# Optimization experiments

Hardware: AMD Instinct MI355X
Metric: run time of the kernel (lower is better)

## Reference

```python
import jax, jax.numpy as jnp
import numpy as np

B, S, D, H = 2, 2048, 1024, 16
DK = D // H  # 64


def rotate_half(x):
    d = x.shape[-1]
    x1, x2 = x[..., : d // 2], x[..., d // 2 :]
    return jnp.concatenate([-x2, x1], axis=-1)


def apply_rope(q, k):
    # q, k: [B, H, S, DK]
    d_k = q.shape[-1]
    seq_len = q.shape[-2]
    theta = 10000.0 ** (-2.0 / d_k * jnp.arange(d_k // 2, dtype=q.dtype))
    positions = jnp.arange(seq_len, dtype=q.dtype)
    angles = jnp.outer(positions, theta)                    # [S, DK/2]
    cos = jnp.tile(jnp.cos(angles), (1, 2))                 # [S, DK]
    sin = jnp.tile(jnp.sin(angles), (1, 2))
    q = q * cos + rotate_half(q) * sin
    k = k * cos + rotate_half(k) * sin
    return q, k


def setup_inputs() -> dict:
    key = jax.random.key(0)
    ks = jax.random.split(key, 9)
    std = 1.0 / np.sqrt(D)
    x = jax.random.normal(ks[0], (B, S, D), dtype=jnp.float32)
    # mask True = masked (code uses masked_fill(mask, -inf)); causal mask
    mask = jnp.triu(jnp.ones((S, S), dtype=bool), k=1)[None, None, :, :]
    mask = jnp.broadcast_to(mask, (B, 1, S, S))
    Wq = jax.random.uniform(ks[1], (D, D), jnp.float32, -std, std)
    bq = jax.random.uniform(ks[2], (D,), jnp.float32, -std, std)
    Wk = jax.random.uniform(ks[3], (D, D), jnp.float32, -std, std)
    bk = jax.random.uniform(ks[4], (D,), jnp.float32, -std, std)
    Wv = jax.random.uniform(ks[5], (D, D), jnp.float32, -std, std)
    bv = jax.random.uniform(ks[6], (D,), jnp.float32, -std, std)
    Wo = jax.random.uniform(ks[7], (D, D), jnp.float32, -std, std)
    bo = jax.random.uniform(ks[8], (D,), jnp.float32, -std, std)
    return {"x": x, "mask": mask, "Wq": Wq, "bq": bq, "Wk": Wk, "bk": bk,
            "Wv": Wv, "bv": bv, "Wo": Wo, "bo": bo}


def reference(x, mask, Wq, bq, Wk, bk, Wv, bv, Wo, bo):
    b, s, d = x.shape
    # projections -> [B, H, S, DK]
    q = (x @ Wq + bq).reshape(b, s, H, DK).transpose(0, 2, 1, 3)
    k = (x @ Wk + bk).reshape(b, s, H, DK).transpose(0, 2, 1, 3)
    v = (x @ Wv + bv).reshape(b, s, H, DK).transpose(0, 2, 1, 3)
    q, k = apply_rope(q, k)
    scores = jnp.einsum("bhqd,bhkd->bhqk", q, k) / np.sqrt(DK)
    scores = jnp.where(mask, -jnp.inf, scores)
    probs = jax.nn.softmax(scores, axis=-1)
    attn = jnp.einsum("bhqk,bhkd->bhqd", probs, v)
    o = attn.transpose(0, 2, 1, 3).reshape(b, s, H * DK)
    return o @ Wo + bo
```

## Files before the change

kernel.cpp:

```cpp
#include <hip/hip_runtime.h>
#include <hip/hip_bf16.h>
#include <math.h>

typedef __hip_bfloat16 bf16;
typedef __attribute__((ext_vector_type(8))) short short8;
typedef __attribute__((ext_vector_type(4))) short s16x4;
typedef __attribute__((ext_vector_type(4))) float f32x4;

#define B_  2
#define S_  2048
#define D_  1024
#define H_  16
#define DK_ 64

#define QSCALE 0.18033688011112043f
#define EXPOFF 11.541560327111707f

__device__ inline short bfs(float f) { return __builtin_bit_cast(short, __float2bfloat16(f)); }

#define GLL16(gptr, lptr)                                                        \
    __builtin_amdgcn_global_load_lds(                                            \
        (const __attribute__((address_space(1))) void*)(gptr),                   \
        (__attribute__((address_space(3))) void*)(lptr), 16, 0, 0)

#if __has_builtin(__builtin_amdgcn_mfma_f32_16x16x16bf16_1k)
#define MFMA_16x16x16(A, Bv, C) __builtin_amdgcn_mfma_f32_16x16x16bf16_1k(A, Bv, C, 0, 0, 0)
#elif __has_builtin(__builtin_amdgcn_mfma_f32_16x16x16_bf16)
#define MFMA_16x16x16(A, Bv, C) __builtin_amdgcn_mfma_f32_16x16x16_bf16(A, Bv, C, 0, 0, 0)
#else
static __device__ inline f32x4 mfma16_asm(s16x4 a, s16x4 b, f32x4 c) {
    f32x4 d;
    asm volatile("v_mfma_f32_16x16x16_bf16 %0, %1, %2, %3\n\ts_nop 7\n\ts_nop 7"
                 : "=v"(d) : "v"(a), "v"(b), "v"(c));
    return d;
}
#define MFMA_16x16x16(A, Bv, C) mfma16_asm(A, Bv, C)
#endif

__global__ __launch_bounds__(256)
void prep_k(const float* __restrict__ x,
            const float* __restrict__ W0, const float* __restrict__ W1,
            const float* __restrict__ W2, const float* __restrict__ W3,
            bf16* __restrict__ cx, bf16* __restrict__ Wt)
{
    const int z = blockIdx.z;
    const int t = threadIdx.x;
    if (z == 4) {
        const int bid = blockIdx.y * 16 + blockIdx.x;
        #pragma unroll
        for (int i = 0; i < 16; i++) {
            const size_t g = ((size_t)bid * 256 + t) * 4 + (size_t)i * 262144;
            const float4 v = *(const float4*)(x + g);
            s16x4 o = { bfs(v.x), bfs(v.y), bfs(v.z), bfs(v.w) };
            *(s16x4*)(cx + g) = o;
        }
        return;
    }
    __shared__ float Lt[64][65];
    const float* W = (z == 0) ? W0 : (z == 1) ? W1 : (z == 2) ? W2 : W3;
    bf16* dst = Wt + (size_t)z * D_ * D_;
    const int k0 = blockIdx.y * 64, n0 = blockIdx.x * 64;
    #pragma unroll
    for (int p = 0; p < 4; p++) {
        const int idx = p * 256 + t;
        const int row = idx >> 4, cb = (idx & 15) * 4;
        const float4 v = *(const float4*)(W + (size_t)(k0 + row) * D_ + n0 + cb);
        Lt[cb + 0][row] = v.x; Lt[cb + 1][row] = v.y;
        Lt[cb + 2][row] = v.z; Lt[cb + 3][row] = v.w;
    }
    __syncthreads();
    #pragma unroll
    for (int p = 0; p < 4; p++) {
        const int idx = p * 256 + t;
        const int n = idx >> 4, kb = (idx & 15) * 4;
        s16x4 o = { bfs(Lt[n][kb]), bfs(Lt[n][kb + 1]), bfs(Lt[n][kb + 2]), bfs(Lt[n][kb + 3]) };
        *(s16x4*)(dst + (size_t)(n0 + n) * D_ + k0 + kb) = o;
    }
}

template<int MODE, int TM>
__global__ __launch_bounds__(256)
void gemm_k(const bf16* __restrict__ A, const bf16* __restrict__ WtAll,
            const float* __restrict__ b0, const float* __restrict__ b1,
            const float* __restrict__ b2,
            bf16* __restrict__ d0, bf16* __restrict__ d1, bf16* __restrict__ d2,
            float* __restrict__ fout)
{
    constexpr int K = D_;
    constexpr int MT = (B_ * S_) / TM;
    constexpr int AI = TM / 64;
    const int L = (int)blockIdx.x;
    const int m0 = (L & (MT - 1)) * TM;
    const int rest = L / MT;
    const int z = (MODE == 0) ? (rest >> 4) : 3;
    const int n0 = (MODE == 0) ? (rest & 15) * 64 : rest * 64;
    const bf16* W = WtAll + (size_t)z * D_ * D_;
    const float* bias = (MODE == 1) ? b0 : ((z == 0) ? b0 : (z == 1) ? b1 : b2);

    __shared__ __align__(16) short As[TM * 32];
    __shared__ __align__(16) short Bs[64 * 32];

    const int t = threadIdx.x;
    const int wave = t >> 6, lane = t & 63, quad = lane >> 4, l16 = lane & 15;
    const int wm = wave * (TM / 4);

    const bf16* gA0 = A + (size_t)(m0 + (t >> 2)) * K + (t & 3) * 8;
    const bf16* gA1 = gA0 + (size_t)64 * K;
    const bf16* gW0 = W + (size_t)(n0 + (t >> 2)) * K + (t & 3) * 8;
    const int wb = wave * 512;

    f32x4 acc[AI][4] = {};

    for (int k0 = 0; k0 < K; k0 += 32) {
        __syncthreads();
        GLL16(gA0 + k0, &As[wb]);
        if (TM == 128) GLL16(gA1 + k0, &As[2048 + wb]);
        GLL16(gW0 + k0, &Bs[wb]);
        __syncthreads();
        short8 af[AI], bf[4];
        #pragma unroll
        for (int i = 0; i < AI; i++) af[i] = *(const short8*)&As[(wm + i * 16 + l16) * 32 + quad * 8];
        #pragma unroll
        for (int j = 0; j < 4; j++) bf[j] = *(const short8*)&Bs[(j * 16 + l16) * 32 + quad * 8];
        #pragma unroll
        for (int i = 0; i < AI; i++)
            #pragma unroll
            for (int j = 0; j < 4; j++)
                acc[i][j] = __builtin_amdgcn_mfma_f32_16x16x32_bf16(af[i], bf[j], acc[i][j], 0, 0, 0);
    }

    if (MODE == 1) {
        #pragma unroll
        for (int j = 0; j < 4; j++) {
            const int ncol = n0 + j * 16 + l16;
            const float bb = bias[ncol];
            #pragma unroll
            for (int i = 0; i < AI; i++) {
                const int mbase = m0 + wm + i * 16 + quad * 4;
                #pragma unroll
                for (int r = 0; r < 4; r++)
                    fout[(size_t)(mbase + r) * D_ + ncol] = acc[i][j][r] + bb;
            }
        }
    } else if (z == 2) {
        const int h = n0 >> 6;
        #pragma unroll
        for (int j = 0; j < 4; j++) {
            const int ncol = n0 + j * 16 + l16;
            const float bb = bias[ncol];
            const int dk = ncol & 63;
            #pragma unroll
            for (int i = 0; i < AI; i++) {
                const int mbase = m0 + wm + i * 16 + quad * 4;
                #pragma unroll
                for (int r = 0; r < 4; r++) {
                    const int m = mbase + r;
                    const int b = m >> 11, s = m & (S_ - 1);
                    d2[(((size_t)(b * H_ + h)) * DK_ + dk) * S_ + s] = __float2bfloat16(acc[i][j][r] + bb);
                }
            }
        }
    } else {
        bf16* dst = z ? d1 : d0;
        const float sc = z ? 1.0f : QSCALE;
        const int h = n0 >> 6;
        #pragma unroll
        for (int j = 0; j < 2; j++) {
            const int dk = j * 16 + l16;
            const float th = exp2f((float)dk * -0.41524101186092029f);
            const float blo = bias[(h << 6) + dk];
            const float bhi = bias[(h << 6) + dk + 32];
            #pragma unroll
            for (int i = 0; i < AI; i++) {
                #pragma unroll
                for (int r = 0; r < 4; r++) {
                    const int m = m0 + wm + i * 16 + quad * 4 + r;
                    const int b = m >> 11, s = m & (S_ - 1);
                    float sn, cs;
                    sincosf((float)s * th, &sn, &cs);
                    const float v1 = acc[i][j][r] + blo;
                    const float v2 = acc[i][j + 2][r] + bhi;
                    bf16* p = dst + (((size_t)(b * H_ + h)) * S_ + s) * DK_;
                    p[dk]      = __float2bfloat16((v1 * cs - v2 * sn) * sc);
                    p[dk + 32] = __float2bfloat16((v2 * cs + v1 * sn) * sc);
                }
            }
        }
    }
}

template<bool DIAG>
__device__ __forceinline__
void attn_tile(const short* __restrict__ Ks, const short* __restrict__ Vts,
               const short8 qf0, const short8 qf1,
               f32x4* ot, float& l_acc,
               const int wave, const int quad, const int l16)
{
    const int kkmax = DIAG ? wave : 3;
    #pragma unroll
    for (int kk = 0; kk <= kkmax; kk++) {
        const short8 kf0 = *(const short8*)&Ks[(kk * 16 + l16) * 72 + quad * 8];
        const short8 kf1 = *(const short8*)&Ks[(kk * 16 + l16) * 72 + 32 + quad * 8];
        f32x4 st = {};
        st = __builtin_amdgcn_mfma_f32_16x16x32_bf16(kf0, qf0, st, 0, 0, 0);
        st = __builtin_amdgcn_mfma_f32_16x16x32_bf16(kf1, qf1, st, 0, 0, 0);

        s16x4 pt;
        float psum = 0.0f;
        #pragma unroll
        for (int r = 0; r < 4; r++) {
            float p;
            if (DIAG) {
                const bool masked = (kk == wave) && (quad * 4 + r > l16);
                p = masked ? 0.0f : exp2f(st[r] - EXPOFF);
            } else {
                p = exp2f(st[r] - EXPOFF);
            }
            psum += p;
            pt[r] = bfs(p);
        }
        l_acc += psum;

        #pragma unroll
        for (int dt = 0; dt < 4; dt++) {
            const s16x4 vf = *(const s16x4*)&Vts[(dt * 16 + l16) * 72 + kk * 16 + quad * 4];
            ot[dt] = MFMA_16x16x16(vf, pt, ot[dt]);
        }
    }
}

__global__ __launch_bounds__(256)
void attn_k(const bf16* __restrict__ q_ws, const bf16* __restrict__ k_ws,
            const bf16* __restrict__ vt_ws, bf16* __restrict__ attn_ws)
{
    __shared__ __align__(16) short Ks[2][64 * 72];
    __shared__ __align__(16) short Vts[2][64 * 72];

    const int linear = (int)blockIdx.y * 16 + (int)blockIdx.x;
    const int bh = linear & 31;
    const int pr = linear >> 5;
    const int qtA = pr, qtB = 31 - pr;
    const int t = threadIdx.x;
    const int wave = t >> 6, quad = (t & 63) >> 4, l16 = t & 15;
    const bf16* Kb = k_ws + (size_t)bh * S_ * DK_;
    const bf16* Vb = vt_ws + (size_t)bh * DK_ * S_;
    const int b = bh >> 4, h = bh & 15;

    const bf16* QbA = q_ws + ((size_t)bh * S_ + qtA * 64 + wave * 16) * DK_;
    const bf16* QbB = q_ws + ((size_t)bh * S_ + qtB * 64 + wave * 16) * DK_;
    const short8 qfA0 = *(const short8*)(QbA + (size_t)l16 * DK_ + quad * 8);
    const short8 qfA1 = *(const short8*)(QbA + (size_t)l16 * DK_ + 32 + quad * 8);
    const short8 qfB0 = *(const short8*)(QbB + (size_t)l16 * DK_ + quad * 8);
    const short8 qfB1 = *(const short8*)(QbB + (size_t)l16 * DK_ + 32 + quad * 8);

    float lA = 0.0f, lB = 0.0f;
    f32x4 otA[4] = {}, otB[4] = {};

    for (int kt0 = 0; kt0 <= qtB; kt0 += 2) {
        const int kt1 = kt0 + 1;
        const bool has1 = (kt1 <= qtB);
        __syncthreads();
        #pragma unroll
        for (int p = 0; p < 2; p++) {
            const int idx = p * 256 + t;
            const int row = idx >> 3, cb = (idx & 7) * 8;
            *(float4*)&Ks[0][row * 72 + cb]  = *(const float4*)(Kb + (size_t)(kt0 * 64 + row) * DK_ + cb);
            *(float4*)&Vts[0][row * 72 + cb] = *(const float4*)(Vb + (size_t)row * S_ + kt0 * 64 + cb);
        }
        if (has1) {
            #pragma unroll
            for (int p = 0; p < 2; p++) {
                const int idx = p * 256 + t;
                const int row = idx >> 3, cb = (idx & 7) * 8;
                *(float4*)&Ks[1][row * 72 + cb]  = *(const float4*)(Kb + (size_t)(kt1 * 64 + row) * DK_ + cb);
                *(float4*)&Vts[1][row * 72 + cb] = *(const float4*)(Vb + (size_t)row * S_ + kt1 * 64 + cb);
            }
        }
        __syncthreads();

        if (kt0 == qtB) attn_tile<true >(Ks[0], Vts[0], qfB0, qfB1, otB, lB, wave, quad, l16);
        else            attn_tile<false>(Ks[0], Vts[0], qfB0, qfB1, otB, lB, wave, quad, l16);
        if (has1) {
            if (kt1 == qtB) attn_tile<true >(Ks[1], Vts[1], qfB0, qfB1, otB, lB, wave, quad, l16);
            else            attn_tile<false>(Ks[1], Vts[1], qfB0, qfB1, otB, lB, wave, quad, l16);
        }
        if (kt0 <= qtA) {
            if (kt0 == qtA) attn_tile<true >(Ks[0], Vts[0], qfA0, qfA1, otA, lA, wave, quad, l16);
            else            attn_tile<false>(Ks[0], Vts[0], qfA0, qfA1, otA, lA, wave, quad, l16);
        }
        if (has1 && kt1 <= qtA) {
            if (kt1 == qtA) attn_tile<true >(Ks[1], Vts[1], qfA0, qfA1, otA, lA, wave, quad, l16);
            else            attn_tile<false>(Ks[1], Vts[1], qfA0, qfA1, otA, lA, wave, quad, l16);
        }
    }

    #pragma unroll
    for (int which = 0; which < 2; which++) {
        float l_acc = which ? lB : lA;
        f32x4* ot = which ? otB : otA;
        const int q0 = (which ? qtB : qtA) * 64;
        l_acc += __shfl_xor(l_acc, 16, 64);
        l_acc += __shfl_xor(l_acc, 32, 64);
        const float inv = 1.0f / l_acc;
        const int srow = q0 + wave * 16 + l16;
        bf16* orow = attn_ws + ((size_t)(b * S_ + srow)) * D_ + h * 64;
        #pragma unroll
        for (int dt = 0; dt < 4; dt++) {
            s16x4 o4 = { bfs(ot[dt][0] * inv), bfs(ot[dt][1] * inv),
                         bfs(ot[dt][2] * inv), bfs(ot[dt][3] * inv) };
            *(s16x4*)(orow + dt * 16 + quad * 4) = o4;
        }
    }
}

extern "C" void kernel_launch(void* const* d_in, const int* in_sizes, int n_in,
                              void* d_out, int out_size, void* d_ws, size_t ws_size,
                              hipStream_t stream)
{
    (void)out_size; (void)ws_size;
    const float* x = nullptr;
    const float* W[4] = {nullptr, nullptr, nullptr, nullptr};
    const float* bias[4] = {nullptr, nullptr, nullptr, nullptr};
    int wi = 0, bi = 0;
    for (int i = 0; i < n_in; i++) {
        const int sz = in_sizes[i];
        if (sz == B_ * S_ * D_ && x == nullptr) x = (const float*)d_in[i];
        else if (sz == D_ * D_ && wi < 4) W[wi++] = (const float*)d_in[i];
        else if (sz == D_ && bi < 4) bias[bi++] = (const float*)d_in[i];
    }

    bf16* ws = (bf16*)d_ws;
    const size_t SEG = (size_t)B_ * S_ * D_;
    bf16* canonX  = ws;
    bf16* Wt      = ws + SEG;
    bf16* k_ws    = ws + 2 * SEG;
    bf16* vt_ws   = ws + 3 * SEG;
    bf16* attn_ws = canonX;
    bf16* q_ws    = (bf16*)d_out;

    prep_k<<<dim3(16, 16, 5), 256, 0, stream>>>(x, W[0], W[1], W[2], W[3], canonX, Wt);

    gemm_k<0, 128><<<dim3(1536, 1, 1), 256, 0, stream>>>(
        canonX, Wt, bias[0], bias[1], bias[2], q_ws, k_ws, vt_ws, nullptr);

    attn_k<<<dim3(16, 32), 256, 0, stream>>>(q_ws, k_ws, vt_ws, attn_ws);

    gemm_k<1, 64><<<dim3(1024, 1, 1), 256, 0, stream>>>(
        attn_ws, Wt, bias[3], nullptr, nullptr, nullptr, nullptr, nullptr,
        (float*)d_out);
}
```

Baseline: 218.6 us.

## Retile GEMMs to 128xTN blocks and split attention into one q-tile per block

The projection GEMM now uses 128x128 tiles, with waves arranged 2x2 so each wave covers one head. The output GEMM uses 128x64 tiles, which halves the grid sizes and improves operand reuse per block. The attention kernel drops the paired q-tile scheme and gives each block a single q-tile. It orders tiles longest-first within groups, with bh on blockIdx.x. This doubles the attention grid to raise parallelism, but each block now loads K/V for only one query tile, so K/V reuse drops and the scheduler must balance the causal load.

```diff
diff --git a/kernel.cpp b/kernel.cpp
--- a/kernel.cpp
+++ b/kernel.cpp
@@ -78,7 +78,7 @@
     }
 }
 
-template<int MODE, int TM>
+template<int MODE, int TN>
 __global__ __launch_bounds__(256)
 void gemm_k(const bf16* __restrict__ A, const bf16* __restrict__ WtAll,
             const float* __restrict__ b0, const float* __restrict__ b1,
@@ -87,25 +87,30 @@
             float* __restrict__ fout)
 {
     constexpr int K = D_;
+    constexpr int TM = 128;
     constexpr int MT = (B_ * S_) / TM;
-    constexpr int AI = TM / 64;
+    constexpr int NT = D_ / TN;
+    constexpr int WAVES_N = TN / 64;
+    constexpr int WM = TM / (4 / WAVES_N);
+    constexpr int AI = WM / 16;
+
     const int L = (int)blockIdx.x;
     const int m0 = (L & (MT - 1)) * TM;
-    const int rest = L / MT;
-    const int z = (MODE == 0) ? (rest >> 4) : 3;
-    const int n0 = (MODE == 0) ? (rest & 15) * 64 : rest * 64;
+    const int rest = L >> 5;
+    const int z = (MODE == 0) ? (rest >> 3) : 3;
+    const int n0 = (MODE == 0) ? (rest & (NT - 1)) * TN : rest * TN;
     const bf16* W = WtAll + (size_t)z * D_ * D_;
     const float* bias = (MODE == 1) ? b0 : ((z == 0) ? b0 : (z == 1) ? b1 : b2);
 
     __shared__ __align__(16) short As[TM * 32];
-    __shared__ __align__(16) short Bs[64 * 32];
+    __shared__ __align__(16) short Bs[TN * 32];
 
     const int t = threadIdx.x;
     const int wave = t >> 6, lane = t & 63, quad = lane >> 4, l16 = lane & 15;
-    const int wm = wave * (TM / 4);
+    const int wr = (WAVES_N == 2) ? (wave >> 1) : wave;
+    const int wc = (WAVES_N == 2) ? (wave & 1) : 0;
 
     const bf16* gA0 = A + (size_t)(m0 + (t >> 2)) * K + (t & 3) * 8;
-    const bf16* gA1 = gA0 + (size_t)64 * K;
     const bf16* gW0 = W + (size_t)(n0 + (t >> 2)) * K + (t & 3) * 8;
     const int wb = wave * 512;
 
@@ -114,44 +119,44 @@
     for (int k0 = 0; k0 < K; k0 += 32) {
         __syncthreads();
         GLL16(gA0 + k0, &As[wb]);
-        if (TM == 128) GLL16(gA1 + k0, &As[2048 + wb]);
+        GLL16(gA0 + (size_t)64 * K + k0, &As[2048 + wb]);
         GLL16(gW0 + k0, &Bs[wb]);
+        if (TN == 128) GLL16(gW0 + (size_t)64 * K + k0, &Bs[2048 + wb]);
         __syncthreads();
-        short8 af[AI], bf[4];
-        #pragma unroll
-        for (int i = 0; i < AI; i++) af[i] = *(const short8*)&As[(wm + i * 16 + l16) * 32 + quad * 8];
-        #pragma unroll
-        for (int j = 0; j < 4; j++) bf[j] = *(const short8*)&Bs[(j * 16 + l16) * 32 + quad * 8];
+        short8 af[AI], bfv[4];
+        #pragma unroll
+        for (int i = 0; i < AI; i++) af[i] = *(const short8*)&As[(wr * WM + i * 16 + l16) * 32 + quad * 8];
+        #pragma unroll
+        for (int j = 0; j < 4; j++) bfv[j] = *(const short8*)&Bs[(wc * 64 + j * 16 + l16) * 32 + quad * 8];
         #pragma unroll
         for (int i = 0; i < AI; i++)
             #pragma unroll
             for (int j = 0; j < 4; j++)
-                acc[i][j] = __builtin_amdgcn_mfma_f32_16x16x32_bf16(af[i], bf[j], acc[i][j], 0, 0, 0);
+                acc[i][j] = __builtin_amdgcn_mfma_f32_16x16x32_bf16(af[i], bfv[j], acc[i][j], 0, 0, 0);
     }
 
     if (MODE == 1) {
         #pragma unroll
         for (int j = 0; j < 4; j++) {
-            const int ncol = n0 + j * 16 + l16;
+            const int ncol = n0 + wc * 64 + j * 16 + l16;
             const float bb = bias[ncol];
             #pragma unroll
             for (int i = 0; i < AI; i++) {
-                const int mbase = m0 + wm + i * 16 + quad * 4;
+                const int mbase = m0 + wr * WM + i * 16 + quad * 4;
                 #pragma unroll
                 for (int r = 0; r < 4; r++)
                     fout[(size_t)(mbase + r) * D_ + ncol] = acc[i][j][r] + bb;
             }
         }
     } else if (z == 2) {
-        const int h = n0 >> 6;
+        const int h = (n0 >> 6) + wc;
         #pragma unroll
         for (int j = 0; j < 4; j++) {
-            const int ncol = n0 + j * 16 + l16;
-            const float bb = bias[ncol];
-            const int dk = ncol & 63;
+            const int dk = j * 16 + l16;
+            const float bb = bias[(h << 6) + dk];
             #pragma unroll
             for (int i = 0; i < AI; i++) {
-                const int mbase = m0 + wm + i * 16 + quad * 4;
+                const int mbase = m0 + wr * WM + i * 16 + quad * 4;
                 #pragma unroll
                 for (int r = 0; r < 4; r++) {
                     const int m = mbase + r;
@@ -163,7 +168,7 @@
     } else {
         bf16* dst = z ? d1 : d0;
         const float sc = z ? 1.0f : QSCALE;
-        const int h = n0 >> 6;
+        const int h = (n0 >> 6) + wc;
         #pragma unroll
         for (int j = 0; j < 2; j++) {
             const int dk = j * 16 + l16;
@@ -174,7 +179,7 @@
             for (int i = 0; i < AI; i++) {
                 #pragma unroll
                 for (int r = 0; r < 4; r++) {
-                    const int m = m0 + wm + i * 16 + quad * 4 + r;
+                    const int m = m0 + wr * WM + i * 16 + quad * 4 + r;
                     const int b = m >> 11, s = m & (S_ - 1);
                     float sn, cs;
                     sincosf((float)s * th, &sn, &cs);
@@ -236,29 +241,27 @@
     __shared__ __align__(16) short Ks[2][64 * 72];
     __shared__ __align__(16) short Vts[2][64 * 72];
 
-    const int linear = (int)blockIdx.y * 16 + (int)blockIdx.x;
-    const int bh = linear & 31;
-    const int pr = linear >> 5;
-    const int qtA = pr, qtB = 31 - pr;
+    const int bh = (int)blockIdx.x;
+    const int by = (int)blockIdx.y;
+    const int j8 = by & 7, g = by >> 3;
+    const int qt = (g == 0) ? (31 - j8) : (g == 1) ? j8 : (g == 2) ? (23 - j8) : (8 + j8);
+
     const int t = threadIdx.x;
     const int wave = t >> 6, quad = (t & 63) >> 4, l16 = t & 15;
     const bf16* Kb = k_ws + (size_t)bh * S_ * DK_;
     const bf16* Vb = vt_ws + (size_t)bh * DK_ * S_;
     const int b = bh >> 4, h = bh & 15;
 
-    const bf16* QbA = q_ws + ((size_t)bh * S_ + qtA * 64 + wave * 16) * DK_;
-    const bf16* QbB = q_ws + ((size_t)bh * S_ + qtB * 64 + wave * 16) * DK_;
-    const short8 qfA0 = *(const short8*)(QbA + (size_t)l16 * DK_ + quad * 8);
-    const short8 qfA1 = *(const short8*)(QbA + (size_t)l16 * DK_ + 32 + quad * 8);
-    const short8 qfB0 = *(const short8*)(QbB + (size_t)l16 * DK_ + quad * 8);
-    const short8 qfB1 = *(const short8*)(QbB + (size_t)l16 * DK_ + 32 + quad * 8);
-
-    float lA = 0.0f, lB = 0.0f;
-    f32x4 otA[4] = {}, otB[4] = {};
-
-    for (int kt0 = 0; kt0 <= qtB; kt0 += 2) {
+    const bf16* Qb = q_ws + ((size_t)bh * S_ + qt * 64 + wave * 16) * DK_;
+    const short8 qf0 = *(const short8*)(Qb + (size_t)l16 * DK_ + quad * 8);
+    const short8 qf1 = *(const short8*)(Qb + (size_t)l16 * DK_ + 32 + quad * 8);
+
+    float l_acc = 0.0f;
+    f32x4 ot[4] = {};
+
+    for (int kt0 = 0; kt0 <= qt; kt0 += 2) {
         const int kt1 = kt0 + 1;
-        const bool has1 = (kt1 <= qtB);
+        const bool has1 = (kt1 <= qt);
         __syncthreads();
         #pragma unroll
         for (int p = 0; p < 2; p++) {
@@ -278,38 +281,24 @@
         }
         __syncthreads();
 
-        if (kt0 == qtB) attn_tile<true >(Ks[0], Vts[0], qfB0, qfB1, otB, lB, wave, quad, l16);
-        else            attn_tile<false>(Ks[0], Vts[0], qfB0, qfB1, otB, lB, wave, quad, l16);
+        if (kt0 == qt) attn_tile<true >(Ks[0], Vts[0], qf0, qf1, ot, l_acc, wave, quad, l16);
+        else           attn_tile<false>(Ks[0], Vts[0], qf0, qf1, ot, l_acc, wave, quad, l16);
         if (has1) {
-            if (kt1 == qtB) attn_tile<true >(Ks[1], Vts[1], qfB0, qfB1, otB, lB, wave, quad, l16);
-            else            attn_tile<false>(Ks[1], Vts[1], qfB0, qfB1, otB, lB, wave, quad, l16);
-        }
-        if (kt0 <= qtA) {
-            if (kt0 == qtA) attn_tile<true >(Ks[0], Vts[0], qfA0, qfA1, otA, lA, wave, quad, l16);
-            else            attn_tile<false>(Ks[0], Vts[0], qfA0, qfA1, otA, lA, wave, quad, l16);
-        }
-        if (has1 && kt1 <= qtA) {
-            if (kt1 == qtA) attn_tile<true >(Ks[1], Vts[1], qfA0, qfA1, otA, lA, wave, quad, l16);
-            else            attn_tile<false>(Ks[1], Vts[1], qfA0, qfA1, otA, lA, wave, quad, l16);
-        }
-    }
-
+            if (kt1 == qt) attn_tile<true >(Ks[1], Vts[1], qf0, qf1, ot, l_acc, wave, quad, l16);
+            else           attn_tile<false>(Ks[1], Vts[1], qf0, qf1, ot, l_acc, wave, quad, l16);
+        }
+    }
+
+    l_acc += __shfl_xor(l_acc, 16, 64);
+    l_acc += __shfl_xor(l_acc, 32, 64);
+    const float inv = 1.0f / l_acc;
+    const int srow = qt * 64 + wave * 16 + l16;
+    bf16* orow = attn_ws + ((size_t)(b * S_ + srow)) * D_ + h * 64;
     #pragma unroll
-    for (int which = 0; which < 2; which++) {
-        float l_acc = which ? lB : lA;
-        f32x4* ot = which ? otB : otA;
-        const int q0 = (which ? qtB : qtA) * 64;
-        l_acc += __shfl_xor(l_acc, 16, 64);
-        l_acc += __shfl_xor(l_acc, 32, 64);
-        const float inv = 1.0f / l_acc;
-        const int srow = q0 + wave * 16 + l16;
-        bf16* orow = attn_ws + ((size_t)(b * S_ + srow)) * D_ + h * 64;
-        #pragma unroll
-        for (int dt = 0; dt < 4; dt++) {
-            s16x4 o4 = { bfs(ot[dt][0] * inv), bfs(ot[dt][1] * inv),
-                         bfs(ot[dt][2] * inv), bfs(ot[dt][3] * inv) };
-            *(s16x4*)(orow + dt * 16 + quad * 4) = o4;
-        }
+    for (int dt = 0; dt < 4; dt++) {
+        s16x4 o4 = { bfs(ot[dt][0] * inv), bfs(ot[dt][1] * inv),
+                     bfs(ot[dt][2] * inv), bfs(ot[dt][3] * inv) };
+        *(s16x4*)(orow + dt * 16 + quad * 4) = o4;
     }
 }
 
@@ -340,12 +329,12 @@
 
     prep_k<<<dim3(16, 16, 5), 256, 0, stream>>>(x, W[0], W[1], W[2], W[3], canonX, Wt);
 
-    gemm_k<0, 128><<<dim3(1536, 1, 1), 256, 0, stream>>>(
+    gemm_k<0, 128><<<dim3(768, 1, 1), 256, 0, stream>>>(
         canonX, Wt, bias[0], bias[1], bias[2], q_ws, k_ws, vt_ws, nullptr);
 
-    attn_k<<<dim3(16, 32), 256, 0, stream>>>(q_ws, k_ws, vt_ws, attn_ws);
-
-    gemm_k<1, 64><<<dim3(1024, 1, 1), 256, 0, stream>>>(
+    attn_k<<<dim3(32, 32), 256, 0, stream>>>(q_ws, k_ws, vt_ws, attn_ws);
+
+    gemm_k<1, 64><<<dim3(512, 1, 1), 256, 0, stream>>>(
         attn_ws, Wt, bias[3], nullptr, nullptr, nullptr, nullptr, nullptr,
         (float*)d_out);
 }
```

Result: no change. 219.8 us (+0.6%).

## Split attention work across waves by key subtile with LDS cross-wave reduction

Applied to the files above, without the earlier changes.

The attention kernel previously paired two query tiles per block, with each wave owning 16 query rows and walking all 64 keys of each key tile. Now each block handles one query tile, and each wave owns a 16-key slice of every key tile while computing against all 64 query rows. Partial outputs and row sums are then reduced across waves through shared memory. The grid doubles to 1024 blocks and query tiles are ordered so long and short blocks interleave. This should give more parallelism and balanced diagonal masking, at the cost of four times the accumulator registers per wave and an extra LDS reduction pass.

```diff
diff --git a/kernel.cpp b/kernel.cpp
--- a/kernel.cpp
+++ b/kernel.cpp
@@ -117,16 +117,16 @@
         if (TM == 128) GLL16(gA1 + k0, &As[2048 + wb]);
         GLL16(gW0 + k0, &Bs[wb]);
         __syncthreads();
-        short8 af[AI], bf[4];
+        short8 af[AI], bfv[4];
         #pragma unroll
         for (int i = 0; i < AI; i++) af[i] = *(const short8*)&As[(wm + i * 16 + l16) * 32 + quad * 8];
         #pragma unroll
-        for (int j = 0; j < 4; j++) bf[j] = *(const short8*)&Bs[(j * 16 + l16) * 32 + quad * 8];
+        for (int j = 0; j < 4; j++) bfv[j] = *(const short8*)&Bs[(j * 16 + l16) * 32 + quad * 8];
         #pragma unroll
         for (int i = 0; i < AI; i++)
             #pragma unroll
             for (int j = 0; j < 4; j++)
-                acc[i][j] = __builtin_amdgcn_mfma_f32_16x16x32_bf16(af[i], bf[j], acc[i][j], 0, 0, 0);
+                acc[i][j] = __builtin_amdgcn_mfma_f32_16x16x32_bf16(af[i], bfv[j], acc[i][j], 0, 0, 0);
     }
 
     if (MODE == 1) {
@@ -191,19 +191,24 @@
 
 template<bool DIAG>
 __device__ __forceinline__
-void attn_tile(const short* __restrict__ Ks, const short* __restrict__ Vts,
-               const short8 qf0, const short8 qf1,
-               f32x4* ot, float& l_acc,
-               const int wave, const int quad, const int l16)
-{
-    const int kkmax = DIAG ? wave : 3;
-    #pragma unroll
-    for (int kk = 0; kk <= kkmax; kk++) {
-        const short8 kf0 = *(const short8*)&Ks[(kk * 16 + l16) * 72 + quad * 8];
-        const short8 kf1 = *(const short8*)&Ks[(kk * 16 + l16) * 72 + 32 + quad * 8];
+void attn_tile_ks(const short* __restrict__ Ks, const short* __restrict__ Vts,
+                  const short8* qf, f32x4 (&ot)[4][4], float (&l_acc)[4],
+                  const int wave, const int quad, const int l16)
+{
+    const int kb = wave * 16;
+    const short8 kf0 = *(const short8*)&Ks[(kb + l16) * 72 + quad * 8];
+    const short8 kf1 = *(const short8*)&Ks[(kb + l16) * 72 + 32 + quad * 8];
+    s16x4 vf[4];
+    #pragma unroll
+    for (int dt = 0; dt < 4; dt++)
+        vf[dt] = *(const s16x4*)&Vts[(dt * 16 + l16) * 72 + kb + quad * 4];
+
+    #pragma unroll
+    for (int qs = 0; qs < 4; qs++) {
+        if (DIAG && qs < wave) continue;
         f32x4 st = {};
-        st = __builtin_amdgcn_mfma_f32_16x16x32_bf16(kf0, qf0, st, 0, 0, 0);
-        st = __builtin_amdgcn_mfma_f32_16x16x32_bf16(kf1, qf1, st, 0, 0, 0);
+        st = __builtin_amdgcn_mfma_f32_16x16x32_bf16(kf0, qf[qs * 2 + 0], st, 0, 0, 0);
+        st = __builtin_amdgcn_mfma_f32_16x16x32_bf16(kf1, qf[qs * 2 + 1], st, 0, 0, 0);
 
         s16x4 pt;
         float psum = 0.0f;
@@ -211,7 +216,7 @@
         for (int r = 0; r < 4; r++) {
             float p;
             if (DIAG) {
-                const bool masked = (kk == wave) && (quad * 4 + r > l16);
+                const bool masked = (qs == wave) && (quad * 4 + r > l16);
                 p = masked ? 0.0f : exp2f(st[r] - EXPOFF);
             } else {
                 p = exp2f(st[r] - EXPOFF);
@@ -219,13 +224,11 @@
             psum += p;
             pt[r] = bfs(p);
         }
-        l_acc += psum;
-
-        #pragma unroll
-        for (int dt = 0; dt < 4; dt++) {
-            const s16x4 vf = *(const s16x4*)&Vts[(dt * 16 + l16) * 72 + kk * 16 + quad * 4];
-            ot[dt] = MFMA_16x16x16(vf, pt, ot[dt]);
-        }
+        l_acc[qs] += psum;
+
+        #pragma unroll
+        for (int dt = 0; dt < 4; dt++)
+            ot[qs][dt] = MFMA_16x16x16(vf[dt], pt, ot[qs][dt]);
     }
 }
 
@@ -233,83 +236,109 @@
 void attn_k(const bf16* __restrict__ q_ws, const bf16* __restrict__ k_ws,
             const bf16* __restrict__ vt_ws, bf16* __restrict__ attn_ws)
 {
-    __shared__ __align__(16) short Ks[2][64 * 72];
-    __shared__ __align__(16) short Vts[2][64 * 72];
-
-    const int linear = (int)blockIdx.y * 16 + (int)blockIdx.x;
-    const int bh = linear & 31;
-    const int pr = linear >> 5;
-    const int qtA = pr, qtB = 31 - pr;
+    __shared__ __align__(16) short smem[4][64 * 72];
+
+    const int bh = (int)blockIdx.x;
+    const int by = (int)blockIdx.y;
+    const int j8 = by & 7, g = by >> 3;
+    const int qt = (g == 0) ? (31 - j8) : (g == 1) ? j8 : (g == 2) ? (23 - j8) : (8 + j8);
+
     const int t = threadIdx.x;
     const int wave = t >> 6, quad = (t & 63) >> 4, l16 = t & 15;
     const bf16* Kb = k_ws + (size_t)bh * S_ * DK_;
     const bf16* Vb = vt_ws + (size_t)bh * DK_ * S_;
     const int b = bh >> 4, h = bh & 15;
 
-    const bf16* QbA = q_ws + ((size_t)bh * S_ + qtA * 64 + wave * 16) * DK_;
-    const bf16* QbB = q_ws + ((size_t)bh * S_ + qtB * 64 + wave * 16) * DK_;
-    const short8 qfA0 = *(const short8*)(QbA + (size_t)l16 * DK_ + quad * 8);
-    const short8 qfA1 = *(const short8*)(QbA + (size_t)l16 * DK_ + 32 + quad * 8);
-    const short8 qfB0 = *(const short8*)(QbB + (size_t)l16 * DK_ + quad * 8);
-    const short8 qfB1 = *(const short8*)(QbB + (size_t)l16 * DK_ + 32 + quad * 8);
-
-    float lA = 0.0f, lB = 0.0f;
-    f32x4 otA[4] = {}, otB[4] = {};
-
-    for (int kt0 = 0; kt0 <= qtB; kt0 += 2) {
+    const bf16* Qb = q_ws + ((size_t)bh * S_ + qt * 64) * DK_;
+    short8 qf[8];
+    #pragma unroll
+    for (int qs = 0; qs < 4; qs++) {
+        qf[qs * 2 + 0] = *(const short8*)(Qb + (size_t)(qs * 16 + l16) * DK_ + quad * 8);
+        qf[qs * 2 + 1] = *(const short8*)(Qb + (size_t)(qs * 16 + l16) * DK_ + 32 + quad * 8);
+    }
+
+    float l_acc[4] = {0.f, 0.f, 0.f, 0.f};
+    f32x4 ot[4][4] = {};
+
+    for (int kt0 = 0; kt0 <= qt; kt0 += 2) {
         const int kt1 = kt0 + 1;
-        const bool has1 = (kt1 <= qtB);
+        const bool has1 = (kt1 <= qt);
         __syncthreads();
         #pragma unroll
         for (int p = 0; p < 2; p++) {
             const int idx = p * 256 + t;
             const int row = idx >> 3, cb = (idx & 7) * 8;
-            *(float4*)&Ks[0][row * 72 + cb]  = *(const float4*)(Kb + (size_t)(kt0 * 64 + row) * DK_ + cb);
-            *(float4*)&Vts[0][row * 72 + cb] = *(const float4*)(Vb + (size_t)row * S_ + kt0 * 64 + cb);
+            *(float4*)&smem[0][row * 72 + cb] = *(const float4*)(Kb + (size_t)(kt0 * 64 + row) * DK_ + cb);
+            *(float4*)&smem[2][row * 72 + cb] = *(const float4*)(Vb + (size_t)row * S_ + kt0 * 64 + cb);
         }
         if (has1) {
             #pragma unroll
             for (int p = 0; p < 2; p++) {
                 const int idx = p * 256 + t;
                 const int row = idx >> 3, cb = (idx & 7) * 8;
-                *(float4*)&Ks[1][row * 72 + cb]  = *(const float4*)(Kb + (size_t)(kt1 * 64 + row) * DK_ + cb);
-                *(float4*)&Vts[1][row * 72 + cb] = *(const float4*)(Vb + (size_t)row * S_ + kt1 * 64 + cb);
-            }
-        }
-        __syncthreads();
-
-        if (kt0 == qtB) attn_tile<true >(Ks[0], Vts[0], qfB0, qfB1, otB, lB, wave, quad, l16);
-        else            attn_tile<false>(Ks[0], Vts[0], qfB0, qfB1, otB, lB, wave, quad, l16);
+                *(float4*)&smem[1][row * 72 + cb] = *(const float4*)(Kb + (size_t)(kt1 * 64 + row) * DK_ + cb);
+                *(float4*)&smem[3][row * 72 + cb] = *(const float4*)(Vb + (size_t)row * S_ + kt1 * 64 + cb);
+            }
+        }
+        __syncthreads();
+
+        if (kt0 == qt) attn_tile_ks<true >(smem[0], smem[2], qf, ot, l_acc, wave, quad, l16);
+        else           attn_tile_ks<false>(smem[0], smem[2], qf, ot, l_acc, wave, quad, l16);
         if (has1) {
-            if (kt1 == qtB) attn_tile<true >(Ks[1], Vts[1], qfB0, qfB1, otB, lB, wave, quad, l16);
-            else            attn_tile<false>(Ks[1], Vts[1], qfB0, qfB1, otB, lB, wave, quad, l16);
-        }
-        if (kt0 <= qtA) {
-            if (kt0 == qtA) attn_tile<true >(Ks[0], Vts[0], qfA0, qfA1, otA, lA, wave, quad, l16);
-            else            attn_tile<false>(Ks[0], Vts[0], qfA0, qfA1, otA, lA, wave, quad, l16);
-        }
-        if (has1 && kt1 <= qtA) {
-            if (kt1 == qtA) attn_tile<true >(Ks[1], Vts[1], qfA0, qfA1, otA, lA, wave, quad, l16);
-            else            attn_tile<false>(Ks[1], Vts[1], qfA0, qfA1, otA, lA, wave, quad, l16);
-        }
-    }
-
-    #pragma unroll
-    for (int which = 0; which < 2; which++) {
-        float l_acc = which ? lB : lA;
-        f32x4* ot = which ? otB : otA;
-        const int q0 = (which ? qtB : qtA) * 64;
-        l_acc += __shfl_xor(l_acc, 16, 64);
-        l_acc += __shfl_xor(l_acc, 32, 64);
-        const float inv = 1.0f / l_acc;
-        const int srow = q0 + wave * 16 + l16;
-        bf16* orow = attn_ws + ((size_t)(b * S_ + srow)) * D_ + h * 64;
-        #pragma unroll
-        for (int dt = 0; dt < 4; dt++) {
-            s16x4 o4 = { bfs(ot[dt][0] * inv), bfs(ot[dt][1] * inv),
-                         bfs(ot[dt][2] * inv), bfs(ot[dt][3] * inv) };
-            *(s16x4*)(orow + dt * 16 + quad * 4) = o4;
-        }
+            if (kt1 == qt) attn_tile_ks<true >(smem[1], smem[3], qf, ot, l_acc, wave, quad, l16);
+            else           attn_tile_ks<false>(smem[1], smem[3], qf, ot, l_acc, wave, quad, l16);
+        }
+    }
+
+    #pragma unroll
+    for (int qs = 0; qs < 4; qs++) {
+        l_acc[qs] += __shfl_xor(l_acc[qs], 16, 64);
+        l_acc[qs] += __shfl_xor(l_acc[qs], 32, 64);
+    }
+
+    __syncthreads();
+    float* Obuf = (float*)&smem[0][0];
+    float* lred = Obuf + 128 * 68;
+
+    if (quad == 0) {
+        #pragma unroll
+        for (int qs = 0; qs < 4; qs++) lred[wave * 64 + qs * 16 + l16] = l_acc[qs];
+    }
+
+    const int srow0 = qt * 64;
+    #pragma unroll
+    for (int pass = 0; pass < 2; pass++) {
+        if (pass) __syncthreads();
+        #pragma unroll
+        for (int q2 = 0; q2 < 2; q2++) {
+            const int qs = pass * 2 + q2;
+            #pragma unroll
+            for (int dt = 0; dt < 4; dt++) {
+                float* dst = &Obuf[((wave * 2 + q2) * 16 + l16) * 68 + dt * 16 + quad * 4];
+                *(f32x4*)dst = ot[qs][dt];
+            }
+        }
+        __syncthreads();
+        const int g0 = t * 2;
+        const int row = g0 >> 4;
+        const int dq = (g0 & 15) * 4;
+        const int q2r = row >> 4, l16r = row & 15;
+        f32x4 sa = {}, sb = {};
+        float lsum = 0.0f;
+        #pragma unroll
+        for (int w = 0; w < 4; w++) {
+            const float* src = &Obuf[((w * 2 + q2r) * 16 + l16r) * 68 + dq];
+            sa += *(const f32x4*)src;
+            sb += *(const f32x4*)(src + 4);
+            lsum += lred[w * 64 + pass * 32 + row];
+        }
+        const float inv = 1.0f / lsum;
+        const int srow = srow0 + pass * 32 + row;
+        bf16* op = attn_ws + ((size_t)(b * S_ + srow)) * D_ + h * 64 + dq;
+        s16x4 o0 = { bfs(sa[0] * inv), bfs(sa[1] * inv), bfs(sa[2] * inv), bfs(sa[3] * inv) };
+        s16x4 o1 = { bfs(sb[0] * inv), bfs(sb[1] * inv), bfs(sb[2] * inv), bfs(sb[3] * inv) };
+        *(s16x4*)op       = o0;
+        *(s16x4*)(op + 4) = o1;
     }
 }
 
@@ -343,7 +372,7 @@
     gemm_k<0, 128><<<dim3(1536, 1, 1), 256, 0, stream>>>(
         canonX, Wt, bias[0], bias[1], bias[2], q_ws, k_ws, vt_ws, nullptr);
 
-    attn_k<<<dim3(16, 32), 256, 0, stream>>>(q_ws, k_ws, vt_ws, attn_ws);
+    attn_k<<<dim3(32, 32), 256, 0, stream>>>(q_ws, k_ws, vt_ws, attn_ws);
 
     gemm_k<1, 64><<<dim3(1024, 1, 1), 256, 0, stream>>>(
         attn_ws, Wt, bias[3], nullptr, nullptr, nullptr, nullptr, nullptr,
```

New measurement: 225.9 us. +3.3%, slower.

## Split paired attention q-tiles into one q-tile per block with heavy-first ordering

Applied to the files above, without the earlier changes.

The attention kernel previously paired a short and a long causal q-tile in each block (512 blocks) and shared loaded K/V tiles between them. It now launches 1024 blocks, each handling a single q-tile. blockIdx.y is mapped so the longest tiles are dispatched early for load balance. This doubles parallelism and cuts per-block registers and LDS, but K/V tiles are loaded once per q-tile rather than shared across the pair. A GEMM variable is also renamed.

```diff
diff --git a/kernel.cpp b/kernel.cpp
--- a/kernel.cpp
+++ b/kernel.cpp
@@ -117,16 +117,16 @@
         if (TM == 128) GLL16(gA1 + k0, &As[2048 + wb]);
         GLL16(gW0 + k0, &Bs[wb]);
         __syncthreads();
-        short8 af[AI], bf[4];
+        short8 af[AI], bfv[4];
         #pragma unroll
         for (int i = 0; i < AI; i++) af[i] = *(const short8*)&As[(wm + i * 16 + l16) * 32 + quad * 8];
         #pragma unroll
-        for (int j = 0; j < 4; j++) bf[j] = *(const short8*)&Bs[(j * 16 + l16) * 32 + quad * 8];
+        for (int j = 0; j < 4; j++) bfv[j] = *(const short8*)&Bs[(j * 16 + l16) * 32 + quad * 8];
         #pragma unroll
         for (int i = 0; i < AI; i++)
             #pragma unroll
             for (int j = 0; j < 4; j++)
-                acc[i][j] = __builtin_amdgcn_mfma_f32_16x16x32_bf16(af[i], bf[j], acc[i][j], 0, 0, 0);
+                acc[i][j] = __builtin_amdgcn_mfma_f32_16x16x32_bf16(af[i], bfv[j], acc[i][j], 0, 0, 0);
     }
 
     if (MODE == 1) {
@@ -233,83 +233,52 @@
 void attn_k(const bf16* __restrict__ q_ws, const bf16* __restrict__ k_ws,
             const bf16* __restrict__ vt_ws, bf16* __restrict__ attn_ws)
 {
-    __shared__ __align__(16) short Ks[2][64 * 72];
-    __shared__ __align__(16) short Vts[2][64 * 72];
-
-    const int linear = (int)blockIdx.y * 16 + (int)blockIdx.x;
-    const int bh = linear & 31;
-    const int pr = linear >> 5;
-    const int qtA = pr, qtB = 31 - pr;
+    __shared__ __align__(16) short Ks[64 * 72];
+    __shared__ __align__(16) short Vts[64 * 72];
+
+    const int bh = (int)blockIdx.x;
+    const int by = (int)blockIdx.y;
+    const int j8 = by & 7, g = by >> 3;
+    const int qt = (g == 0) ? (31 - j8) : (g == 1) ? j8 : (g == 2) ? (23 - j8) : (8 + j8);
+
     const int t = threadIdx.x;
     const int wave = t >> 6, quad = (t & 63) >> 4, l16 = t & 15;
     const bf16* Kb = k_ws + (size_t)bh * S_ * DK_;
     const bf16* Vb = vt_ws + (size_t)bh * DK_ * S_;
     const int b = bh >> 4, h = bh & 15;
 
-    const bf16* QbA = q_ws + ((size_t)bh * S_ + qtA * 64 + wave * 16) * DK_;
-    const bf16* QbB = q_ws + ((size_t)bh * S_ + qtB * 64 + wave * 16) * DK_;
-    const short8 qfA0 = *(const short8*)(QbA + (size_t)l16 * DK_ + quad * 8);
-    const short8 qfA1 = *(const short8*)(QbA + (size_t)l16 * DK_ + 32 + quad * 8);
-    const short8 qfB0 = *(const short8*)(QbB + (size_t)l16 * DK_ + quad * 8);
-    const short8 qfB1 = *(const short8*)(QbB + (size_t)l16 * DK_ + 32 + quad * 8);
-
-    float lA = 0.0f, lB = 0.0f;
-    f32x4 otA[4] = {}, otB[4] = {};
-
-    for (int kt0 = 0; kt0 <= qtB; kt0 += 2) {
-        const int kt1 = kt0 + 1;
-        const bool has1 = (kt1 <= qtB);
+    const bf16* Qb = q_ws + ((size_t)bh * S_ + qt * 64 + wave * 16) * DK_;
+    const short8 qf0 = *(const short8*)(Qb + (size_t)l16 * DK_ + quad * 8);
+    const short8 qf1 = *(const short8*)(Qb + (size_t)l16 * DK_ + 32 + quad * 8);
+
+    float l_acc = 0.0f;
+    f32x4 ot[4] = {};
+
+    for (int kt = 0; kt <= qt; kt++) {
         __syncthreads();
         #pragma unroll
         for (int p = 0; p < 2; p++) {
             const int idx = p * 256 + t;
             const int row = idx >> 3, cb = (idx & 7) * 8;
-            *(float4*)&Ks[0][row * 72 + cb]  = *(const float4*)(Kb + (size_t)(kt0 * 64 + row) * DK_ + cb);
-            *(float4*)&Vts[0][row * 72 + cb] = *(const float4*)(Vb + (size_t)row * S_ + kt0 * 64 + cb);
-        }
-        if (has1) {
-            #pragma unroll
-            for (int p = 0; p < 2; p++) {
-                const int idx = p * 256 + t;
-                const int row = idx >> 3, cb = (idx & 7) * 8;
-                *(float4*)&Ks[1][row * 72 + cb]  = *(const float4*)(Kb + (size_t)(kt1 * 64 + row) * DK_ + cb);
-                *(float4*)&Vts[1][row * 72 + cb] = *(const float4*)(Vb + (size_t)row * S_ + kt1 * 64 + cb);
-            }
+            *(float4*)&Ks[row * 72 + cb]  = *(const float4*)(Kb + (size_t)(kt * 64 + row) * DK_ + cb);
+            *(float4*)&Vts[row * 72 + cb] = *(const float4*)(Vb + (size_t)row * S_ + kt * 64 + cb);
         }
         __syncthreads();
 
-        if (kt0 == qtB) attn_tile<true >(Ks[0], Vts[0], qfB0, qfB1, otB, lB, wave, quad, l16);
-        else            attn_tile<false>(Ks[0], Vts[0], qfB0, qfB1, otB, lB, wave, quad, l16);
-        if (has1) {
-            if (kt1 == qtB) attn_tile<true >(Ks[1], Vts[1], qfB0, qfB1, otB, lB, wave, quad, l16);
-            else            attn_tile<false>(Ks[1], Vts[1], qfB0, qfB1, otB, lB, wave, quad, l16);
-        }
-        if (kt0 <= qtA) {
-            if (kt0 == qtA) attn_tile<true >(Ks[0], Vts[0], qfA0, qfA1, otA, lA, wave, quad, l16);
-            else            attn_tile<false>(Ks[0], Vts[0], qfA0, qfA1, otA, lA, wave, quad, l16);
-        }
-        if (has1 && kt1 <= qtA) {
-            if (kt1 == qtA) attn_tile<true >(Ks[1], Vts[1], qfA0, qfA1, otA, lA, wave, quad, l16);
-            else            attn_tile<false>(Ks[1], Vts[1], qfA0, qfA1, otA, lA, wave, quad, l16);
-        }
-    }
-
+        if (kt == qt) attn_tile<true >(Ks, Vts, qf0, qf1, ot, l_acc, wave, quad, l16);
+        else          attn_tile<false>(Ks, Vts, qf0, qf1, ot, l_acc, wave, quad, l16);
+    }
+
+    l_acc += __shfl_xor(l_acc, 16, 64);
+    l_acc += __shfl_xor(l_acc, 32, 64);
+    const float inv = 1.0f / l_acc;
+    const int srow = qt * 64 + wave * 16 + l16;
+    bf16* orow = attn_ws + ((size_t)(b * S_ + srow)) * D_ + h * 64;
     #pragma unroll
-    for (int which = 0; which < 2; which++) {
-        float l_acc = which ? lB : lA;
-        f32x4* ot = which ? otB : otA;
-        const int q0 = (which ? qtB : qtA) * 64;
-        l_acc += __shfl_xor(l_acc, 16, 64);
-        l_acc += __shfl_xor(l_acc, 32, 64);
-        const float inv = 1.0f / l_acc;
-        const int srow = q0 + wave * 16 + l16;
-        bf16* orow = attn_ws + ((size_t)(b * S_ + srow)) * D_ + h * 64;
-        #pragma unroll
-        for (int dt = 0; dt < 4; dt++) {
-            s16x4 o4 = { bfs(ot[dt][0] * inv), bfs(ot[dt][1] * inv),
-                         bfs(ot[dt][2] * inv), bfs(ot[dt][3] * inv) };
-            *(s16x4*)(orow + dt * 16 + quad * 4) = o4;
-        }
+    for (int dt = 0; dt < 4; dt++) {
+        s16x4 o4 = { bfs(ot[dt][0] * inv), bfs(ot[dt][1] * inv),
+                     bfs(ot[dt][2] * inv), bfs(ot[dt][3] * inv) };
+        *(s16x4*)(orow + dt * 16 + quad * 4) = o4;
     }
 }
 
@@ -343,7 +312,7 @@
     gemm_k<0, 128><<<dim3(1536, 1, 1), 256, 0, stream>>>(
         canonX, Wt, bias[0], bias[1], bias[2], q_ws, k_ws, vt_ws, nullptr);
 
-    attn_k<<<dim3(16, 32), 256, 0, stream>>>(q_ws, k_ws, vt_ws, attn_ws);
+    attn_k<<<dim3(32, 32), 256, 0, stream>>>(q_ws, k_ws, vt_ws, attn_ws);
 
     gemm_k<1, 64><<<dim3(1024, 1, 1), 256, 0, stream>>>(
         attn_ws, Wt, bias[3], nullptr, nullptr, nullptr, nullptr, nullptr,
```

Result: no change. 217.5 us (-0.5%).
